# Optimization experiments

Hardware: AMD Instinct MI355X
Metric: run time of the kernel (lower is better)

## Reference

```python
import jax, jax.numpy as jnp
import numpy as np

N_NODES = 50000
N_FEAT = 32
HIDDEN = 64
K_HOPS = 3
N_EDGES = 800000
BN_EPS = 1e-5


def setup_inputs() -> dict:
    key = jax.random.key(0)
    ks = jax.random.split(key, 16)
    x = jax.random.normal(ks[0], (N_NODES, N_FEAT), jnp.float32)
    edge_index = jax.random.randint(ks[1], (2, N_EDGES), 0, N_NODES, jnp.int32)
    edge_weight = jax.random.uniform(ks[2], (N_EDGES,), jnp.float32, minval=0.1, maxval=1.0)
    fin = N_FEAT + HIDDEN  # DCRNN cell concatenates [X, H]
    s = 1.0 / np.sqrt(fin)
    Wz = jax.random.uniform(ks[3], (2, K_HOPS, fin, HIDDEN), jnp.float32, -s, s)
    Wr = jax.random.uniform(ks[4], (2, K_HOPS, fin, HIDDEN), jnp.float32, -s, s)
    Wh = jax.random.uniform(ks[5], (2, K_HOPS, fin, HIDDEN), jnp.float32, -s, s)
    bz = jax.random.uniform(ks[6], (HIDDEN,), jnp.float32, -s, s)
    br = jax.random.uniform(ks[7], (HIDDEN,), jnp.float32, -s, s)
    bh = jax.random.uniform(ks[8], (HIDDEN,), jnp.float32, -s, s)
    g = 1.0 / np.sqrt(HIDDEN)
    gcn_w = jax.random.uniform(ks[9], (HIDDEN, HIDDEN), jnp.float32, -g, g)
    gcn_b = jax.random.uniform(ks[10], (HIDDEN,), jnp.float32, -g, g)
    bn_gamma = jnp.ones((HIDDEN,), jnp.float32)
    bn_beta = jnp.zeros((HIDDEN,), jnp.float32)
    lin_w = jax.random.uniform(ks[11], (HIDDEN, 1), jnp.float32, -g, g)
    lin_b = jax.random.uniform(ks[12], (1,), jnp.float32, -g, g)
    return dict(x=x, edge_index=edge_index, edge_weight=edge_weight,
                Wz=Wz, bz=bz, Wr=Wr, br=br, Wh=Wh, bh=bh,
                gcn_w=gcn_w, gcn_b=gcn_b, bn_gamma=bn_gamma, bn_beta=bn_beta,
                lin_w=lin_w, lin_b=lin_b)


def _dconv(X, W, b, row, col, ew, do_inv, di_inv, n):
    # Diffusion conv: H = sum_k T_out^k(X) @ W[0,k] + T_in^k(X) @ W[1,k] + b
    # T_out: propagate along edges (source -> target), out-degree normalized
    # T_in : propagate along reversed edges, in-degree normalized
    H = X @ W[0, 0] + X @ W[1, 0]
    Tx_o = X
    Tx_i = X
    w_out = (ew * do_inv[row])[:, None]  # [E,1]
    w_in = (ew * di_inv[col])[:, None]   # [E,1]
    for k in range(1, W.shape[1]):
        Tx_o = jax.ops.segment_sum(w_out * Tx_o[row], col, num_segments=n)
        Tx_i = jax.ops.segment_sum(w_in * Tx_i[col], row, num_segments=n)
        H = H + Tx_o @ W[0, k] + Tx_i @ W[1, k]
    return H + b


def reference(x, edge_index, edge_weight, Wz, bz, Wr, br, Wh, bh,
              gcn_w, gcn_b, bn_gamma, bn_beta, lin_w, lin_b):
    n = x.shape[0]
    row, col = edge_index[0], edge_index[1]
    # weighted degrees (as in DConv's dense-adjacency degree computation)
    deg_out = jax.ops.segment_sum(edge_weight, row, num_segments=n)
    deg_in = jax.ops.segment_sum(edge_weight, col, num_segments=n)
    do_inv = jnp.where(deg_out > 0, 1.0 / deg_out, 0.0)
    di_inv = jnp.where(deg_in > 0, 1.0 / deg_in, 0.0)

    # --- DCRNN cell (GRU with diffusion convs), hidden state starts at zero ---
    H0 = jnp.zeros((n, Wz.shape[-1]), x.dtype)
    XH = jnp.concatenate([x, H0], axis=1)
    Z = jax.nn.sigmoid(_dconv(XH, Wz, bz, row, col, edge_weight, do_inv, di_inv, n))
    R = jax.nn.sigmoid(_dconv(XH, Wr, br, row, col, edge_weight, do_inv, di_inv, n))
    XHR = jnp.concatenate([x, H0 * R], axis=1)
    H_tilde = jnp.tanh(_dconv(XHR, Wh, bh, row, col, edge_weight, do_inv, di_inv, n))
    H = Z * H0 + (1.0 - Z) * H_tilde  # [N, HIDDEN]

    # --- GCNConv(H, edge_index) with unit edge weights + self loops, sym norm ---
    xw = H @ gcn_w
    ones_e = jnp.ones((row.shape[0],), x.dtype)
    deg = jax.ops.segment_sum(ones_e, col, num_segments=n) + 1.0  # + self loop
    dis = jnp.where(deg > 0, jax.lax.rsqrt(deg), 0.0)
    norm = (dis[row] * dis[col])[:, None]
    y = jax.ops.segment_sum(norm * xw[row], col, num_segments=n) + (dis * dis)[:, None] * xw
    y = y + gcn_b

    # ReLU -> BatchNorm1d (batch statistics, biased var) -> Dropout(identity/eval) -> Linear
    y = jax.nn.relu(y)
    mean = jnp.mean(y, axis=0)
    var = jnp.mean(jnp.square(y - mean), axis=0)
    y = (y - mean) * jax.lax.rsqrt(var + BN_EPS) * bn_gamma + bn_beta
    out = y @ lin_w + lin_b  # [N, 1]
    return out
```

## Files before the change

kernel.cpp:

```cpp
#include <hip/hip_runtime.h>
#include <hip/hip_fp16.h>
#include <math.h>


#define BN_EPS 1e-5f
#define CAPB 6
#define CAP  64
#define ITEMS 2048
#define KI 8
#define REGCAP 5120

typedef _Float16 v8h __attribute__((ext_vector_type(8)));
typedef float v4f __attribute__((ext_vector_type(4)));

__global__ __launch_bounds__(256) void k_sort1(
    const int* __restrict__ row, const int* __restrict__ col,
    const float* __restrict__ ew,
    unsigned long long* __restrict__ bufC, unsigned long long* __restrict__ bufR,
    unsigned* __restrict__ gcnt, int E, int nbk, int reg) {
    __shared__ unsigned hist[256], scanb[256], cur[256], runb[256];
    __shared__ unsigned long long outb[ITEMS];
    int t = threadIdx.x;
    int s = (blockIdx.x >= nbk) ? 1 : 0;
    int blk = blockIdx.x - s * nbk;
    int e0 = blk * ITEMS;
    int vcnt = E - e0; if (vcnt > ITEMS) vcnt = ITEMS;
    hist[t] = 0;
    __syncthreads();
    for (int k = 0; k < KI; ++k) {
        int e = e0 + k * 256 + t;
        if (e < E) {
            int key = s ? row[e] : col[e];
            atomicAdd(&hist[key >> 8], 1u);
        }
    }
    __syncthreads();
    scanb[t] = hist[t];
    __syncthreads();
    for (int off = 1; off < 256; off <<= 1) {
        unsigned v = (t >= off) ? scanb[t - off] : 0u;
        __syncthreads();
        scanb[t] += v;
        __syncthreads();
    }
    unsigned excl = scanb[t] - hist[t];
    __syncthreads();
    scanb[t] = excl;
    cur[t] = excl;
    runb[t] = (unsigned)(t * reg) + atomicAdd(&gcnt[s * 256 + t], hist[t]);
    __syncthreads();
    for (int k = 0; k < KI; ++k) {
        int e = e0 + k * 256 + t;
        if (e < E) {
            int key, oth;
            if (s) { key = row[e]; oth = col[e]; }
            else   { key = col[e]; oth = row[e]; }
            unsigned hw = (unsigned)__half_as_ushort(__float2half(ew[e]));
            unsigned long long it = ((unsigned long long)(unsigned)key << 32)
                                  | ((unsigned)oth << 16) | hw;
            unsigned r = atomicAdd(&cur[key >> 8], 1u);
            outb[r] = it;
        }
    }
    __syncthreads();
    unsigned long long* buf = s ? bufR : bufC;
    for (int k = 0; k < KI; ++k) {
        int idx = k * 256 + t;
        if (idx < vcnt) {
            unsigned long long it = outb[idx];
            unsigned d = (unsigned)(it >> 40) & 255u;
            buf[(size_t)runb[d] + ((unsigned)idx - scanb[d])] = it;
        }
    }
}

__device__ inline float ent_w(unsigned e) {
    return __half2float(__ushort_as_half((unsigned short)(e & 0xffffu)));
}

__global__ __launch_bounds__(256) void k_sort2(
    const unsigned long long* __restrict__ bufC, const unsigned long long* __restrict__ bufR,
    const unsigned* __restrict__ gcnt,
    unsigned* __restrict__ ent_col, unsigned* __restrict__ ent_row,
    int* __restrict__ cnt_col, int* __restrict__ cnt_row,
    float* __restrict__ di_inv, float* __restrict__ do_inv, float* __restrict__ dis,
    int N, int reg, int ndig) {
    __shared__ unsigned hist[256], scanb[256], cur[256];
    __shared__ unsigned outp[REGCAP];
    __shared__ unsigned char outl[REGCAP];
    int t = threadIdx.x;
    int s = (blockIdx.x >= ndig) ? 1 : 0;
    int d0 = blockIdx.x - s * ndig;
    const unsigned long long* src = (s ? bufR : bufC) + (size_t)d0 * reg;
    unsigned* ent = s ? ent_row : ent_col;
    int cin = (int)gcnt[s * 256 + d0]; if (cin > REGCAP) cin = REGCAP;
    hist[t] = 0;
    __syncthreads();
    for (int i = t; i < cin; i += 256) {
        unsigned l = (unsigned)(src[i] >> 32) & 255u;
        atomicAdd(&hist[l], 1u);
    }
    __syncthreads();
    scanb[t] = hist[t];
    __syncthreads();
    for (int off = 1; off < 256; off <<= 1) {
        unsigned v = (t >= off) ? scanb[t - off] : 0u;
        __syncthreads();
        scanb[t] += v;
        __syncthreads();
    }
    unsigned excl = scanb[t] - hist[t];
    __syncthreads();
    scanb[t] = excl;
    cur[t] = excl;
    __syncthreads();
    for (int i = t; i < cin; i += 256) {
        unsigned long long it = src[i];
        unsigned l = (unsigned)(it >> 32) & 255u;
        unsigned r = atomicAdd(&cur[l], 1u);
        outp[r] = (unsigned)it;
        outl[r] = (unsigned char)l;
    }
    __syncthreads();
    int node0 = d0 << 8;
    for (int i = t; i < cin; i += 256) {
        unsigned l = outl[i];
        int slot = i - (int)scanb[l];
        int node = node0 + (int)l;
        if (slot < CAP && node < N)
            ent[((size_t)node << CAPB) + slot] = outp[i];
    }
    int node = node0 + t;
    if (node < N) {
        unsigned beg = scanb[t], n = hist[t];
        float sum = 0.f;
        for (unsigned j = 0; j < n; ++j) sum += ent_w(outp[beg + j]);
        float inv = sum > 0.f ? 1.f / sum : 0.f;
        if (s) { do_inv[node] = inv; cnt_row[node] = (int)n; }
        else   { di_inv[node] = inv; cnt_col[node] = (int)n;
                 dis[node] = rsqrtf((float)n + 1.0f); }
    }
}

__global__ void k_cvt_x(const float* __restrict__ xf, __half* __restrict__ xh, int n2) {
    int t = blockIdx.x * blockDim.x + threadIdx.x;
    if (t >= n2) return;
    float2 v = *(const float2*)(xf + 2 * (size_t)t);
    __half2 h; h.x = __float2half(v.x); h.y = __float2half(v.y);
    *(__half2*)(xh + 2 * (size_t)t) = h;
}

__global__ void k_hop(const unsigned* __restrict__ ent_col, const unsigned* __restrict__ ent_row,
                      const int* __restrict__ cnt_col, const int* __restrict__ cnt_row,
                      const __half2* __restrict__ So, const __half2* __restrict__ Si,
                      const float* __restrict__ do_inv, const float* __restrict__ di_inv,
                      __half2* __restrict__ Do, __half2* __restrict__ Di, int N) {
    int t = blockIdx.x * blockDim.x + threadIdx.x;
    int f = t & 15;
    int p = t >> 4;
    if (p >= 2 * N) return;
    const unsigned* ent; const __half2* S; const float* inv; __half2* D;
    int d, cnt;
    if (p < N) { d = p;     ent = ent_col; S = So; inv = do_inv; D = Do; cnt = min(cnt_col[d], CAP); }
    else       { d = p - N; ent = ent_row; S = Si; inv = di_inv; D = Di; cnt = min(cnt_row[d], CAP); }
    ent += ((size_t)d << CAPB);
    float a0 = 0.f, a1 = 0.f;
    int j = 0;
    for (; j + 7 < cnt; j += 8) {
        unsigned e0 = ent[j],     e1 = ent[j + 1], e2 = ent[j + 2], e3 = ent[j + 3];
        unsigned e4 = ent[j + 4], e5 = ent[j + 5], e6 = ent[j + 6], e7 = ent[j + 7];
        int s0 = e0 >> 16, s1 = e1 >> 16, s2 = e2 >> 16, s3 = e3 >> 16;
        int s4 = e4 >> 16, s5 = e5 >> 16, s6 = e6 >> 16, s7 = e7 >> 16;
        float w0 = ent_w(e0) * inv[s0], w1 = ent_w(e1) * inv[s1];
        float w2 = ent_w(e2) * inv[s2], w3 = ent_w(e3) * inv[s3];
        float w4 = ent_w(e4) * inv[s4], w5 = ent_w(e5) * inv[s5];
        float w6 = ent_w(e6) * inv[s6], w7 = ent_w(e7) * inv[s7];
        float2 v0 = __half22float2(S[(size_t)s0 * 16 + f]);
        float2 v1 = __half22float2(S[(size_t)s1 * 16 + f]);
        float2 v2 = __half22float2(S[(size_t)s2 * 16 + f]);
        float2 v3 = __half22float2(S[(size_t)s3 * 16 + f]);
        float2 v4 = __half22float2(S[(size_t)s4 * 16 + f]);
        float2 v5 = __half22float2(S[(size_t)s5 * 16 + f]);
        float2 v6 = __half22float2(S[(size_t)s6 * 16 + f]);
        float2 v7 = __half22float2(S[(size_t)s7 * 16 + f]);
        a0 += w0 * v0.x + w1 * v1.x + w2 * v2.x + w3 * v3.x
            + w4 * v4.x + w5 * v5.x + w6 * v6.x + w7 * v7.x;
        a1 += w0 * v0.y + w1 * v1.y + w2 * v2.y + w3 * v3.y
            + w4 * v4.y + w5 * v5.y + w6 * v6.y + w7 * v7.y;
    }
    for (; j + 3 < cnt; j += 4) {
        unsigned e0 = ent[j],     e1 = ent[j + 1];
        unsigned e2 = ent[j + 2], e3 = ent[j + 3];
        int s0 = e0 >> 16, s1 = e1 >> 16, s2 = e2 >> 16, s3 = e3 >> 16;
        float w0 = ent_w(e0) * inv[s0], w1 = ent_w(e1) * inv[s1];
        float w2 = ent_w(e2) * inv[s2], w3 = ent_w(e3) * inv[s3];
        float2 v0 = __half22float2(S[(size_t)s0 * 16 + f]);
        float2 v1 = __half22float2(S[(size_t)s1 * 16 + f]);
        float2 v2 = __half22float2(S[(size_t)s2 * 16 + f]);
        float2 v3 = __half22float2(S[(size_t)s3 * 16 + f]);
        a0 += w0 * v0.x + w1 * v1.x + w2 * v2.x + w3 * v3.x;
        a1 += w0 * v0.y + w1 * v1.y + w2 * v2.y + w3 * v3.y;
    }
    for (; j < cnt; ++j) {
        unsigned e0 = ent[j];
        int s0 = e0 >> 16;
        float w0 = ent_w(e0) * inv[s0];
        float2 v0 = __half22float2(S[(size_t)s0 * 16 + f]);
        a0 += w0 * v0.x;
        a1 += w0 * v0.y;
    }
    D[(size_t)d * 16 + f] = __floats2half2_rn(a0, a1);
}

__global__ void k_wprep(const float* __restrict__ Wz, const float* __restrict__ Wh,
                        const float* __restrict__ gcn_w,
                        __half* __restrict__ wzT, __half* __restrict__ whT,
                        __half* __restrict__ gwT) {
    int t = blockIdx.x * blockDim.x + threadIdx.x;
    if (t < 64 * 160) {
        int c = t / 160, k = t % 160;
        int blk = k >> 5, r = k & 31;
        float vz, vh;
        if (blk == 0) {
            vz = Wz[r * 64 + c] + Wz[(288 + r) * 64 + c];
            vh = Wh[r * 64 + c] + Wh[(288 + r) * 64 + c];
        } else {
            int kk = (blk + 1) >> 1, dd = (blk + 1) & 1;
            int off = ((dd * 3 + kk) * 96 + r) * 64 + c;
            vz = Wz[off]; vh = Wh[off];
        }
        wzT[t] = __float2half(vz);
        whT[t] = __float2half(vh);
    }
    if (t < 64 * 64) {
        int c = t >> 6, k = t & 63;
        gwT[t] = __float2half(gcn_w[k * 64 + c]);
    }
}

__device__ inline v8h ldh8(const __half* p) { return *(const v8h*)p; }

__global__ __launch_bounds__(256) void k_zh_mfma(
    const __half* __restrict__ xh, const __half* __restrict__ t1o,
    const __half* __restrict__ t1i, const __half* __restrict__ t2o,
    const __half* __restrict__ t2i,
    const __half* __restrict__ wzT, const __half* __restrict__ whT,
    const float* __restrict__ bz, const float* __restrict__ bh,
    const float* __restrict__ dis, __half* __restrict__ Hd, int N) {
    int lane = threadIdx.x & 63;
    int wv = threadIdx.x >> 6;
    int q = lane >> 4, m = lane & 15;
    int c = wv * 16 + m;
    int ko = q * 8;

    const __half* wz = wzT + c * 160 + ko;
    const __half* wh = whT + c * 160 + ko;
    v8h bz0 = ldh8(wz),       bh0 = ldh8(wh);
    v8h bz1 = ldh8(wz + 32),  bh1 = ldh8(wh + 32);
    v8h bz2 = ldh8(wz + 64),  bh2 = ldh8(wh + 64);
    v8h bz3 = ldh8(wz + 96),  bh3 = ldh8(wh + 96);
    v8h bz4 = ldh8(wz + 128), bh4 = ldh8(wh + 128);
    float bzc = bz[c], bhc = bh[c];

    int T = (N + 15) >> 4;
    for (int t = blockIdx.x; t < T; t += gridDim.x) {
        int n0 = t << 4;
        int nn = n0 + m; if (nn > N - 1) nn = N - 1;
        size_t off = (size_t)nn * 32 + ko;
        v8h a0 = ldh8(xh + off);
        v8h a1 = ldh8(t1o + off);
        v8h a2 = ldh8(t1i + off);
        v8h a3 = ldh8(t2o + off);
        v8h a4 = ldh8(t2i + off);
        v4f az = {0.f, 0.f, 0.f, 0.f}, ah = {0.f, 0.f, 0.f, 0.f};
        az = __builtin_amdgcn_mfma_f32_16x16x32_f16(a0, bz0, az, 0, 0, 0);
        ah = __builtin_amdgcn_mfma_f32_16x16x32_f16(a0, bh0, ah, 0, 0, 0);
        az = __builtin_amdgcn_mfma_f32_16x16x32_f16(a1, bz1, az, 0, 0, 0);
        ah = __builtin_amdgcn_mfma_f32_16x16x32_f16(a1, bh1, ah, 0, 0, 0);
        az = __builtin_amdgcn_mfma_f32_16x16x32_f16(a2, bz2, az, 0, 0, 0);
        ah = __builtin_amdgcn_mfma_f32_16x16x32_f16(a2, bh2, ah, 0, 0, 0);
        az = __builtin_amdgcn_mfma_f32_16x16x32_f16(a3, bz3, az, 0, 0, 0);
        ah = __builtin_amdgcn_mfma_f32_16x16x32_f16(a3, bh3, ah, 0, 0, 0);
        az = __builtin_amdgcn_mfma_f32_16x16x32_f16(a4, bz4, az, 0, 0, 0);
        ah = __builtin_amdgcn_mfma_f32_16x16x32_f16(a4, bh4, ah, 0, 0, 0);

#pragma unroll
        for (int i = 0; i < 4; ++i) {
            float zv = 1.f / (1.f + expf(-(az[i] + bzc)));
            float hv = (1.f - zv) * tanhf(ah[i] + bhc);
            int node = n0 + q * 4 + i;
            if (node < N) Hd[(size_t)node * 64 + c] = __float2half(dis[node] * hv);
        }
    }
}

__global__ __launch_bounds__(256) void k_aggw(
    const unsigned* __restrict__ ent_col, const int* __restrict__ cnt_col,
    const float* __restrict__ dis, const __half* __restrict__ Hd,
    const __half* __restrict__ gwT, const float* __restrict__ gcn_b,
    float* __restrict__ y, float* __restrict__ stats, int N) {
    __shared__ _Float16 Hl[16 * 72];
    __shared__ float red[2][256];
    int lane = threadIdx.x & 63;
    int wv = threadIdx.x >> 6;
    int q = lane >> 4, m = lane & 15;
    int c = wv * 16 + m;
    int ko = q * 8;
    v8h g0 = ldh8(gwT + c * 64 + ko);
    v8h g1 = ldh8(gwT + c * 64 + 32 + ko);
    float bl = gcn_b[c];
    float sa = 0.f, s2a = 0.f;
    int T = (N + 15) >> 4;
    for (int t = blockIdx.x; t < T; t += gridDim.x) {
        int n0 = t << 4;
#pragma unroll
        for (int i = 0; i < 4; ++i) {
            int d = n0 + wv * 4 + i;
            float acc = 0.f;
            if (d < N) {
                acc = __half2float(Hd[(size_t)d * 64 + lane]);
                const unsigned* ent = ent_col + ((size_t)d << CAPB);
                int cnt = min(cnt_col[d], CAP);
                int j = 0;
                for (; j + 7 < cnt; j += 8) {
                    unsigned e0 = ent[j],     e1 = ent[j + 1], e2 = ent[j + 2], e3 = ent[j + 3];
                    unsigned e4 = ent[j + 4], e5 = ent[j + 5], e6 = ent[j + 6], e7 = ent[j + 7];
                    float v0 = __half2float(Hd[(size_t)(e0 >> 16) * 64 + lane]);
                    float v1 = __half2float(Hd[(size_t)(e1 >> 16) * 64 + lane]);
                    float v2 = __half2float(Hd[(size_t)(e2 >> 16) * 64 + lane]);
                    float v3 = __half2float(Hd[(size_t)(e3 >> 16) * 64 + lane]);
                    float v4 = __half2float(Hd[(size_t)(e4 >> 16) * 64 + lane]);
                    float v5 = __half2float(Hd[(size_t)(e5 >> 16) * 64 + lane]);
                    float v6 = __half2float(Hd[(size_t)(e6 >> 16) * 64 + lane]);
                    float v7 = __half2float(Hd[(size_t)(e7 >> 16) * 64 + lane]);
                    acc += (v0 + v1 + v2 + v3) + (v4 + v5 + v6 + v7);
                }
                for (; j + 3 < cnt; j += 4) {
                    unsigned e0 = ent[j],     e1 = ent[j + 1];
                    unsigned e2 = ent[j + 2], e3 = ent[j + 3];
                    float v0 = __half2float(Hd[(size_t)(e0 >> 16) * 64 + lane]);
                    float v1 = __half2float(Hd[(size_t)(e1 >> 16) * 64 + lane]);
                    float v2 = __half2float(Hd[(size_t)(e2 >> 16) * 64 + lane]);
                    float v3 = __half2float(Hd[(size_t)(e3 >> 16) * 64 + lane]);
                    acc += v0 + v1 + v2 + v3;
                }
                for (; j < cnt; ++j)
                    acc += __half2float(Hd[(size_t)(ent[j] >> 16) * 64 + lane]);
                acc *= dis[d];
            }
            Hl[(wv * 4 + i) * 72 + lane] = (_Float16)acc;
        }
        __syncthreads();
        v8h a0 = *(const v8h*)&Hl[m * 72 + ko];
        v8h a1 = *(const v8h*)&Hl[m * 72 + 32 + ko];
        v4f acc = {0.f, 0.f, 0.f, 0.f};
        acc = __builtin_amdgcn_mfma_f32_16x16x32_f16(a0, g0, acc, 0, 0, 0);
        acc = __builtin_amdgcn_mfma_f32_16x16x32_f16(a1, g1, acc, 0, 0, 0);
#pragma unroll
        for (int i = 0; i < 4; ++i) {
            int node = n0 + q * 4 + i;
            if (node < N) {
                float v = acc[i] + bl;
                v = v > 0.f ? v : 0.f;
                y[(size_t)node * 64 + c] = v;
                sa += v; s2a += v * v;
            }
        }
        __syncthreads();
    }
    red[0][threadIdx.x] = sa;
    red[1][threadIdx.x] = s2a;
    __syncthreads();
    if (q == 0) {
        int t0 = threadIdx.x;
        float ts  = red[0][t0] + red[0][t0 + 16] + red[0][t0 + 32] + red[0][t0 + 48];
        float ts2 = red[1][t0] + red[1][t0 + 16] + red[1][t0 + 32] + red[1][t0 + 48];
        atomicAdd(&stats[c], ts);
        atomicAdd(&stats[64 + c], ts2);
    }
}

__global__ void k_final(const float* __restrict__ y, const float* __restrict__ stats,
                        const float* __restrict__ gma, const float* __restrict__ bta,
                        const float* __restrict__ lw, const float* __restrict__ lb,
                        float* __restrict__ out, int N) {
    int lane = threadIdx.x & 63;
    int wave = (blockIdx.x * blockDim.x + threadIdx.x) >> 6;
    if (wave >= N) return;
    float invN = 1.0f / (float)N;
    float mean = stats[lane] * invN;
    float var  = stats[64 + lane] * invN - mean * mean;
    float istd = rsqrtf(var + BN_EPS);
    float v = y[(size_t)wave * 64 + lane];
    float t = (v - mean) * istd * gma[lane] + bta[lane];
    float p = t * lw[lane];
    for (int off = 32; off > 0; off >>= 1)
        p += __shfl_down(p, off, 64);
    if (lane == 0) out[wave] = p + lb[0];
}

extern "C" void kernel_launch(void* const* d_in, const int* in_sizes, int n_in,
                              void* d_out, int out_size, void* d_ws, size_t ws_size,
                              hipStream_t stream) {
    const float* x     = (const float*)d_in[0];
    const int*   ei    = (const int*)d_in[1];
    const float* ew    = (const float*)d_in[2];
    const float* Wz    = (const float*)d_in[3];
    const float* bz    = (const float*)d_in[4];
    const float* Wh    = (const float*)d_in[7];
    const float* bhv   = (const float*)d_in[8];
    const float* gcn_w = (const float*)d_in[9];
    const float* gcn_b = (const float*)d_in[10];
    const float* gma   = (const float*)d_in[11];
    const float* bta   = (const float*)d_in[12];
    const float* lw    = (const float*)d_in[13];
    const float* lb    = (const float*)d_in[14];
    float* out = (float*)d_out;

    const int N = in_sizes[0] / 32;
    const int E = in_sizes[2];
    const int* row = ei;
    const int* col = ei + E;

    float* ws      = (float*)d_ws;
    int*   cnt_col = (int*)ws;
    int*   cnt_row = (int*)(ws + (size_t)N);
    unsigned* gcnt = (unsigned*)(ws + 2 * (size_t)N);
    float* stats   = ws + 2 * (size_t)N + 512;
    size_t Z0      = 2 * (size_t)N + 640;
    float* dis     = ws + Z0;
    float* do_inv  = ws + Z0 + (size_t)N;
    float* di_inv  = ws + Z0 + 2 * (size_t)N;
    __half* xh     = (__half*)(ws + Z0 + 3 * (size_t)N);
    __half* txo1   = (__half*)(ws + Z0 + 19 * (size_t)N);
    __half* txi1   = (__half*)(ws + Z0 + 35 * (size_t)N);
    __half* txo2   = (__half*)(ws + Z0 + 51 * (size_t)N);
    __half* txi2   = (__half*)(ws + Z0 + 67 * (size_t)N);
    unsigned* ent_col = (unsigned*)(ws + Z0 + 83 * (size_t)N);
    unsigned* ent_row = ent_col + ((size_t)N << CAPB);
    __half* wzT    = (__half*)(ws + Z0 + 211 * (size_t)N);
    __half* whT    = wzT + 64 * 160;
    __half* gwT    = whT + 64 * 160;
    unsigned long long* bufC = (unsigned long long*)(ws + Z0 + 211 * (size_t)N + 16384);
    unsigned long long* bufR = bufC + (size_t)256 * REGCAP;

    __half* Hd = (__half*)ent_row;
    float*  yb = (float*)txo1;

    hipMemsetAsync((char*)d_ws + 2 * (size_t)N * sizeof(float), 0,
                   640 * sizeof(float), stream);

    int nbk = (E + ITEMS - 1) / ITEMS;
    int ndig = (N + 255) / 256;
    k_cvt_x<<<(16 * N + 255) / 256, 256, 0, stream>>>(x, xh, 16 * N);
    k_wprep<<<40, 256, 0, stream>>>(Wz, Wh, gcn_w, wzT, whT, gwT);
    k_sort1<<<2 * nbk, 256, 0, stream>>>(row, col, ew, bufC, bufR, gcnt, E, nbk, REGCAP);
    k_sort2<<<2 * ndig, 256, 0, stream>>>(bufC, bufR, gcnt, ent_col, ent_row,
                                          cnt_col, cnt_row, di_inv, do_inv, dis,
                                          N, REGCAP, ndig);

    int bhop = (2 * N * 16 + 255) / 256;
    k_hop<<<bhop, 256, 0, stream>>>(ent_col, ent_row, cnt_col, cnt_row,
                                    (const __half2*)xh, (const __half2*)xh,
                                    do_inv, di_inv,
                                    (__half2*)txo1, (__half2*)txi1, N);
    k_hop<<<bhop, 256, 0, stream>>>(ent_col, ent_row, cnt_col, cnt_row,
                                    (const __half2*)txo1, (const __half2*)txi1,
                                    do_inv, di_inv,
                                    (__half2*)txo2, (__half2*)txi2, N);

    k_zh_mfma<<<1024, 256, 0, stream>>>(xh, txo1, txi1, txo2, txi2,
                                        wzT, whT, bz, bhv, dis, Hd, N);

    k_aggw<<<1024, 256, 0, stream>>>(ent_col, cnt_col, dis, Hd, gwT, gcn_b,
                                     yb, stats, N);
    k_final<<<(N + 3) / 4, 256, 0, stream>>>(yb, stats, gma, bta, lw, lb, out, N);
}
```

Measured before the change: 268.8 us.

## Split GCN aggregation from MFMA projection into separate half2-gather and GEMM kernels

The fused aggregate-plus-matmul kernel is split in two. The first is a gather kernel where 32 threads per node each read a half2, so each node's row is gathered with wider loads and there is no block-level barrier. The second is a GEMM kernel that loads the aggregated rows directly from global memory into MFMA operands, with no shared memory and no __syncthreads. The intent is more memory-level parallelism and less barrier stalling in the irregular gather. The cost is an extra kernel launch and an extra fp16 write and read of the N×64 intermediate, plus workspace buffers reassigned to hold P and y.

```diff
diff --git a/kernel.cpp b/kernel.cpp
--- a/kernel.cpp
+++ b/kernel.cpp
@@ -294,12 +294,56 @@
     }
 }
 
-__global__ __launch_bounds__(256) void k_aggw(
+__global__ __launch_bounds__(256) void k_agg(
     const unsigned* __restrict__ ent_col, const int* __restrict__ cnt_col,
-    const float* __restrict__ dis, const __half* __restrict__ Hd,
-    const __half* __restrict__ gwT, const float* __restrict__ gcn_b,
+    const float* __restrict__ dis, const __half2* __restrict__ Hd,
+    __half2* __restrict__ P, int N) {
+    int t = blockIdx.x * blockDim.x + threadIdx.x;
+    int f = t & 31;
+    int d = t >> 5;
+    if (d >= N) return;
+    const unsigned* ent = ent_col + ((size_t)d << CAPB);
+    int cnt = min(cnt_col[d], CAP);
+    float2 sv = __half22float2(Hd[(size_t)d * 32 + f]);
+    float a0 = sv.x, a1 = sv.y;
+    int j = 0;
+    for (; j + 7 < cnt; j += 8) {
+        unsigned e0 = ent[j],     e1 = ent[j + 1], e2 = ent[j + 2], e3 = ent[j + 3];
+        unsigned e4 = ent[j + 4], e5 = ent[j + 5], e6 = ent[j + 6], e7 = ent[j + 7];
+        float2 v0 = __half22float2(Hd[(size_t)(e0 >> 16) * 32 + f]);
+        float2 v1 = __half22float2(Hd[(size_t)(e1 >> 16) * 32 + f]);
+        float2 v2 = __half22float2(Hd[(size_t)(e2 >> 16) * 32 + f]);
+        float2 v3 = __half22float2(Hd[(size_t)(e3 >> 16) * 32 + f]);
+        float2 v4 = __half22float2(Hd[(size_t)(e4 >> 16) * 32 + f]);
+        float2 v5 = __half22float2(Hd[(size_t)(e5 >> 16) * 32 + f]);
+        float2 v6 = __half22float2(Hd[(size_t)(e6 >> 16) * 32 + f]);
+        float2 v7 = __half22float2(Hd[(size_t)(e7 >> 16) * 32 + f]);
+        a0 += (v0.x + v1.x + v2.x + v3.x) + (v4.x + v5.x + v6.x + v7.x);
+        a1 += (v0.y + v1.y + v2.y + v3.y) + (v4.y + v5.y + v6.y + v7.y);
+    }
+    for (; j + 3 < cnt; j += 4) {
+        unsigned e0 = ent[j],     e1 = ent[j + 1];
+        unsigned e2 = ent[j + 2], e3 = ent[j + 3];
+        float2 v0 = __half22float2(Hd[(size_t)(e0 >> 16) * 32 + f]);
+        float2 v1 = __half22float2(Hd[(size_t)(e1 >> 16) * 32 + f]);
+        float2 v2 = __half22float2(Hd[(size_t)(e2 >> 16) * 32 + f]);
+        float2 v3 = __half22float2(Hd[(size_t)(e3 >> 16) * 32 + f]);
+        a0 += v0.x + v1.x + v2.x + v3.x;
+        a1 += v0.y + v1.y + v2.y + v3.y;
+    }
+    for (; j < cnt; ++j) {
+        float2 v0 = __half22float2(Hd[(size_t)(ent[j] >> 16) * 32 + f]);
+        a0 += v0.x;
+        a1 += v0.y;
+    }
+    float dd = dis[d];
+    P[(size_t)d * 32 + f] = __floats2half2_rn(dd * a0, dd * a1);
+}
+
+__global__ __launch_bounds__(256) void k_gcn2(
+    const __half* __restrict__ P, const __half* __restrict__ gwT,
+    const float* __restrict__ gcn_b,
     float* __restrict__ y, float* __restrict__ stats, int N) {
-    __shared__ _Float16 Hl[16 * 72];
     __shared__ float red[2][256];
     int lane = threadIdx.x & 63;
     int wv = threadIdx.x >> 6;
@@ -313,46 +357,10 @@
     int T = (N + 15) >> 4;
     for (int t = blockIdx.x; t < T; t += gridDim.x) {
         int n0 = t << 4;
-#pragma unroll
-        for (int i = 0; i < 4; ++i) {
-            int d = n0 + wv * 4 + i;
-            float acc = 0.f;
-            if (d < N) {
-                acc = __half2float(Hd[(size_t)d * 64 + lane]);
-                const unsigned* ent = ent_col + ((size_t)d << CAPB);
-                int cnt = min(cnt_col[d], CAP);
-                int j = 0;
-                for (; j + 7 < cnt; j += 8) {
-                    unsigned e0 = ent[j],     e1 = ent[j + 1], e2 = ent[j + 2], e3 = ent[j + 3];
-                    unsigned e4 = ent[j + 4], e5 = ent[j + 5], e6 = ent[j + 6], e7 = ent[j + 7];
-                    float v0 = __half2float(Hd[(size_t)(e0 >> 16) * 64 + lane]);
-                    float v1 = __half2float(Hd[(size_t)(e1 >> 16) * 64 + lane]);
-                    float v2 = __half2float(Hd[(size_t)(e2 >> 16) * 64 + lane]);
-                    float v3 = __half2float(Hd[(size_t)(e3 >> 16) * 64 + lane]);
-                    float v4 = __half2float(Hd[(size_t)(e4 >> 16) * 64 + lane]);
-                    float v5 = __half2float(Hd[(size_t)(e5 >> 16) * 64 + lane]);
-                    float v6 = __half2float(Hd[(size_t)(e6 >> 16) * 64 + lane]);
-                    float v7 = __half2float(Hd[(size_t)(e7 >> 16) * 64 + lane]);
-                    acc += (v0 + v1 + v2 + v3) + (v4 + v5 + v6 + v7);
-                }
-                for (; j + 3 < cnt; j += 4) {
-                    unsigned e0 = ent[j],     e1 = ent[j + 1];
-                    unsigned e2 = ent[j + 2], e3 = ent[j + 3];
-                    float v0 = __half2float(Hd[(size_t)(e0 >> 16) * 64 + lane]);
-                    float v1 = __half2float(Hd[(size_t)(e1 >> 16) * 64 + lane]);
-                    float v2 = __half2float(Hd[(size_t)(e2 >> 16) * 64 + lane]);
-                    float v3 = __half2float(Hd[(size_t)(e3 >> 16) * 64 + lane]);
-                    acc += v0 + v1 + v2 + v3;
-                }
-                for (; j < cnt; ++j)
-                    acc += __half2float(Hd[(size_t)(ent[j] >> 16) * 64 + lane]);
-                acc *= dis[d];
-            }
-            Hl[(wv * 4 + i) * 72 + lane] = (_Float16)acc;
-        }
-        __syncthreads();
-        v8h a0 = *(const v8h*)&Hl[m * 72 + ko];
-        v8h a1 = *(const v8h*)&Hl[m * 72 + 32 + ko];
+        int nn = n0 + m; if (nn > N - 1) nn = N - 1;
+        const __half* pr = P + (size_t)nn * 64;
+        v8h a0 = ldh8(pr + ko);
+        v8h a1 = ldh8(pr + 32 + ko);
         v4f acc = {0.f, 0.f, 0.f, 0.f};
         acc = __builtin_amdgcn_mfma_f32_16x16x32_f16(a0, g0, acc, 0, 0, 0);
         acc = __builtin_amdgcn_mfma_f32_16x16x32_f16(a1, g1, acc, 0, 0, 0);
@@ -366,7 +374,6 @@
                 sa += v; s2a += v * v;
             }
         }
-        __syncthreads();
     }
     red[0][threadIdx.x] = sa;
     red[1][threadIdx.x] = s2a;
@@ -445,7 +452,8 @@
     unsigned long long* bufR = bufC + (size_t)256 * REGCAP;
 
     __half* Hd = (__half*)ent_row;
-    float*  yb = (float*)txo1;
+    __half* P  = (__half*)xh;
+    float*  yb = (float*)ent_col;
 
     hipMemsetAsync((char*)d_ws + 2 * (size_t)N * sizeof(float), 0,
                    640 * sizeof(float), stream);
@@ -472,7 +480,9 @@
     k_zh_mfma<<<1024, 256, 0, stream>>>(xh, txo1, txi1, txo2, txi2,
                                         wzT, whT, bz, bhv, dis, Hd, N);
 
-    k_aggw<<<1024, 256, 0, stream>>>(ent_col, cnt_col, dis, Hd, gwT, gcn_b,
-                                     yb, stats, N);
+    k_agg<<<(32 * N + 255) / 256, 256, 0, stream>>>(ent_col, cnt_col, dis,
+                                                    (const __half2*)Hd,
+                                                    (__half2*)P, N);
+    k_gcn2<<<1024, 256, 0, stream>>>(P, gwT, gcn_b, yb, stats, N);
     k_final<<<(N + 3) / 4, 256, 0, stream>>>(yb, stats, gma, bta, lw, lb, out, N);
 }
```

Measured after the change: 256.7 us. -4.5%, faster.
